# Kernel optimization log

Measured on AMD Instinct MI355X. Metric: run time of the kernel, lower is better.

The kernel has to match this reference:

```python
import jax, jax.numpy as jnp
import numpy as np

B, N, D_IN, H, D_H, D_OUT = 2, 1024, 1024, 16, 64, 1024
NEG = -1e9


def skew_relative(QE_t):
    # QE_t: [B, H, N, 2N-1] -> [B, H, N, N] via the pad/reshape skew trick
    b, h, n = QE_t.shape[0], QE_t.shape[1], QE_t.shape[2]
    x = jnp.pad(QE_t, ((0, 0), (0, 0), (0, 0), (0, 1)))          # [B,H,N,2N]
    x = x.reshape(b, h, -1)                                       # [B,H,2N^2]
    x = jnp.pad(x, ((0, 0), (0, 0), (0, n - 1)))                  # [B,H,(N+1)(2N-1)]
    x = x.reshape(b, h, n + 1, 2 * n - 1)
    return x[:, :, :n, -n:]


def setup_inputs() -> dict:
    key = jax.random.key(0)
    ks = jax.random.split(key, 8)
    x = jax.random.normal(ks[0], (B, N, D_IN), dtype=jnp.float32)
    E_rel = jax.random.normal(ks[1], (2 * N - 1, D_H), dtype=jnp.float32)
    # additive causal mask [1,1,N,N]
    causal = jnp.tril(jnp.ones((N, N), dtype=bool))
    mask = jnp.where(causal, 0.0, NEG).astype(jnp.float32)[None, None]
    s = 1.0 / np.sqrt(D_IN)
    Wq = jax.random.normal(ks[2], (D_IN, H * D_H), dtype=jnp.float32) * s
    Wk = jax.random.normal(ks[3], (D_IN, H * D_H), dtype=jnp.float32) * s
    Wv = jax.random.normal(ks[4], (D_IN, H * D_H), dtype=jnp.float32) * s
    Wo = jax.random.normal(ks[5], (H * D_H, D_OUT), dtype=jnp.float32) * (1.0 / np.sqrt(H * D_H))
    bo = jnp.zeros((D_OUT,), dtype=jnp.float32)
    return {"x": x, "E_rel": E_rel, "mask": mask, "Wq": Wq, "Wk": Wk, "Wv": Wv, "Wo": Wo, "bo": bo}


def reference(x, E_rel, mask, Wq, Wk, Wv, Wo, bo):
    b = x.shape[0]
    scale = 1.0 / np.sqrt(D_H)
    # project and split heads -> [B, H, N, d]
    Q = (x @ Wq).reshape(b, -1, H, D_H).transpose(0, 2, 1, 3)
    K = (x @ Wk).reshape(b, -1, H, D_H).transpose(0, 2, 1, 3)
    V = (x @ Wv).reshape(b, -1, H, D_H).transpose(0, 2, 1, 3)
    attn = jnp.einsum('bhnd,bhmd->bhnm', Q, K)                    # [B,H,N,N]
    QE_t = jnp.einsum('bhnd,rd->bhnr', Q, E_rel)                  # [B,H,N,2N-1]
    attn = (attn + skew_relative(QE_t)) * scale + mask
    attn = jax.nn.softmax(attn, axis=-1)
    out = jnp.einsum('bhnm,bhmd->bhnd', attn, V)                  # [B,H,N,d]
    out = out.transpose(0, 2, 1, 3).reshape(b, -1, H * D_H)
    return out @ Wo + bo  # dropout is identity at inference
```

## Files before the change

kernel.cpp:

```cpp
#include <hip/hip_runtime.h>
#include <cstdint>
#include <cstddef>

typedef __bf16 bf16;
typedef __bf16 bf16x8 __attribute__((ext_vector_type(8)));
typedef float  f32x4  __attribute__((ext_vector_type(4)));

#define MFMA16(a,b,c) __builtin_amdgcn_mfma_f32_16x16x32_bf16((a),(b),(c),0,0,0)

__device__ __forceinline__ void gload_lds16(const bf16* g, bf16* l) {
  __builtin_amdgcn_global_load_lds((__attribute__((address_space(1))) void*)(g),
                                   (__attribute__((address_space(3))) void*)(l),
                                   16, 0, 0);
}

__global__ __launch_bounds__(256) void prep_k(
    const float* __restrict__ x, const float* __restrict__ E,
    const float* __restrict__ W0, const float* __restrict__ W1,
    const float* __restrict__ W2, const float* __restrict__ W3,
    bf16* __restrict__ xb, bf16* __restrict__ Eb, bf16* __restrict__ Wt) {
  __shared__ float t[32][33];
  const int bid = blockIdx.x;
  const int tid = threadIdx.x;
  if (bid < 2176) {
    const bool isx = (bid < 2048);
    const float* src = isx ? x : E;
    bf16* dst = isx ? xb : Eb;
    const int n = isx ? (2048 * 1024) : (2047 * 64);
    const int i = (isx ? bid : (bid - 2048)) * 1024 + tid * 4;
    if (i < n) {
      float4 v = *(const float4*)(src + i);
      dst[i + 0] = (bf16)v.x;
      dst[i + 1] = (bf16)v.y;
      dst[i + 2] = (bf16)v.z;
      dst[i + 3] = (bf16)v.w;
    }
  } else {
    const int tt = bid - 2176;
    const int z = tt >> 10;
    const int rem = tt & 1023;
    const int cx = (rem & 31) * 32;
    const int ry = (rem >> 5) * 32;
    const float* src = (z == 0) ? W0 : (z == 1) ? W1 : (z == 2) ? W2 : W3;
    bf16* dst = Wt + (size_t)z * (1024 * 1024);
    const int xx = tid & 31, yy = tid >> 5;
    #pragma unroll
    for (int j = 0; j < 32; j += 8) t[yy + j][xx] = src[(size_t)(ry + yy + j) * 1024 + cx + xx];
    __syncthreads();
    #pragma unroll
    for (int j = 0; j < 32; j += 8)
      dst[(size_t)(cx + yy + j) * 1024 + ry + xx] = (bf16)t[xx][yy + j];
  }
}

template <int NI>
__global__ __launch_bounds__(256) void gemm_k(
    const bf16* __restrict__ A, const bf16* __restrict__ Bt,
    bf16* __restrict__ QKV, float* __restrict__ Of,
    const float* __restrict__ bias, const int mode) {
  constexpr int K = 1024;
  const int row0 = blockIdx.x * 64;
  const int col0 = blockIdx.y * (NI * 64);

  __shared__ bf16 As[2][64 * 64];
  __shared__ bf16 Bs[2][NI * 64 * 64];

  const int tid = threadIdx.x;
  const int lane = tid & 63;
  const int wid = tid >> 6;
  const int lr = lane & 15;
  const int g  = lane >> 4;
  const int srow = lane >> 3;
  const int scol = ((lane & 7) ^ srow) * 8;

  f32x4 acc[4][NI];
  #pragma unroll
  for (int a = 0; a < 4; ++a)
    #pragma unroll
    for (int b = 0; b < NI; ++b) acc[a][b] = (f32x4){0.f, 0.f, 0.f, 0.f};

  auto stg = [&](int bb, int k0_) {
    #pragma unroll
    for (int q = 0; q < 2; ++q)
      gload_lds16(A + (size_t)(row0 + wid * 16 + q * 8 + srow) * K + k0_ + scol,
                  &As[bb][(wid * 16 + q * 8) * 64]);
    #pragma unroll
    for (int q = 0; q < 2 * NI; ++q)
      gload_lds16(Bt + (size_t)(col0 + wid * NI * 16 + q * 8 + srow) * K + k0_ + scol,
                  &Bs[bb][(wid * NI * 16 + q * 8) * 64]);
  };

  stg(0, 0);
  for (int t = 0; t < K / 64; ++t) {
    __syncthreads();
    if (t + 1 < K / 64) stg((t + 1) & 1, (t + 1) * 64);
    const bf16* as = &As[t & 1][0];
    const bf16* bs = &Bs[t & 1][0];
    bf16x8 af[4][2], bfv[NI][2];
    #pragma unroll
    for (int mi = 0; mi < 4; ++mi)
      #pragma unroll
      for (int kk = 0; kk < 2; ++kk)
        af[mi][kk] = *(const bf16x8*)&as[(mi * 16 + lr) * 64 + ((kk * 32 + g * 8) ^ ((lr & 7) << 3))];
    #pragma unroll
    for (int ni = 0; ni < NI; ++ni)
      #pragma unroll
      for (int kk = 0; kk < 2; ++kk)
        bfv[ni][kk] = *(const bf16x8*)&bs[(wid * NI * 16 + ni * 16 + lr) * 64 +
                                          ((kk * 32 + g * 8) ^ ((lr & 7) << 3))];
    #pragma unroll
    for (int mi = 0; mi < 4; ++mi)
      #pragma unroll
      for (int ni = 0; ni < NI; ++ni)
        #pragma unroll
        for (int kk = 0; kk < 2; ++kk)
          acc[mi][ni] = MFMA16(af[mi][kk], bfv[ni][kk], acc[mi][ni]);
  }

  #pragma unroll
  for (int mi = 0; mi < 4; ++mi) {
    #pragma unroll
    for (int ni = 0; ni < NI; ++ni) {
      #pragma unroll
      for (int r = 0; r < 4; ++r) {
        const int row = row0 + mi * 16 + g * 4 + r;
        const int col = col0 + wid * NI * 16 + ni * 16 + lr;
        const float v = acc[mi][ni][r];
        if (mode == 2) {
          Of[(size_t)row * 1024 + col] = v + bias[col];
        } else {
          const int b = row >> 10, i = row & 1023;
          const int which = col >> 10, cc = col & 1023;
          const int h = cc >> 6, d = cc & 63;
          if (which < 2)
            QKV[(size_t)which * 2097152 + (((size_t)(b * 16 + h)) * 1024 + i) * 64 + d] = (bf16)v;
          else
            QKV[(size_t)2 * 2097152 + (((size_t)(b * 16 + h)) * 64 + d) * 1024 + i] = (bf16)v;
        }
      }
    }
  }
}

__device__ const int CH_QB[36] = {7,7,7,7,7,7,7, 6,6,6,6,6,6, 5,5,5,5,5, 4,4,4,4,
                                  3,3,3, 2,2, 1, 0,1,2,3,4,5,6,7};
__device__ const int CH_K0[36] = {0,2,4,6,8,10,12, 0,2,4,6,8,10, 0,2,4,6,8, 0,2,4,6,
                                  0,2,4, 0,2, 0, 0,2,4,6,8,10,12,14};
__device__ const int QB_P0[8] = {0,1,3,6,10,15,21,28};

__global__ __launch_bounds__(512, 6) void attn_kernel(
    const bf16* __restrict__ Qh, const bf16* __restrict__ Kh,
    const bf16* __restrict__ Vt, const bf16* __restrict__ Eb,
    bf16* __restrict__ OP, float* __restrict__ LP) {
  constexpr int N = 1024;
  const int flat = blockIdx.y * 36 + blockIdx.x;
  const int task = (flat & 7) * 144 + (flat >> 3);
  const int bh = task / 36;
  const int ch = task - bh * 36;
  const int qb = CH_QB[ch];
  const int kb0 = CH_K0[ch];
  const int i0 = qb * 128;

  const bf16* Qp = Qh + (size_t)bh * N * 64;
  const bf16* Kp = Kh + (size_t)bh * N * 64;
  const bf16* Vp = Vt + (size_t)bh * 64 * N;

  __shared__ bf16 Ks[64 * 64];
  __shared__ bf16 Vs[64 * 64];
  __shared__ bf16 Es[192 * 64];

  const int tid = threadIdx.x;
  const int lane = tid & 63;
  const int wid = tid >> 6;
  const int lr = lane & 15;
  const int g  = lane >> 4;
  const int iw0 = i0 + wid * 16;
  bf16* pp = &Es[(wid * 16) * 64];

  const int srow8 = lane >> 3;
  const int sch = ((lane & 7) ^ srow8) * 8;

  bf16x8 qf[2];
  {
    const bf16* qrow = Qp + (size_t)(iw0 + lr) * 64 + g * 8;
    qf[0] = *(const bf16x8*)(qrow);
    qf[1] = *(const bf16x8*)(qrow + 32);
  }

  float lb[4] = {0.f, 0.f, 0.f, 0.f};
  f32x4 oacc[4];
  #pragma unroll
  for (int r = 0; r < 4; ++r) oacc[r] = (f32x4){0.f, 0.f, 0.f, 0.f};

  constexpr float SC = 0.18033688f;
  const int fb = 7 - wid;

  auto STAGE = [&](int j0) {
    gload_lds16(Kp + (size_t)(j0 + wid * 8 + srow8) * 64 + sch, &Ks[(wid * 8) * 64]);
    gload_lds16(Vp + (size_t)(wid * 8 + srow8) * 1024 + j0 + sch, &Vs[(wid * 8) * 64]);
    const int ebase = (N - 128) + j0 - i0;
    #pragma unroll
    for (int q = 0; q < 3; ++q)
      gload_lds16(Eb + (size_t)(ebase + wid * 24 + q * 8 + srow8) * 64 + sch,
                  &Es[(wid * 24 + q * 8) * 64]);
  };

  STAGE(kb0 * 64);
  __syncthreads();

  #pragma unroll
  for (int t = 0; t < 2; ++t) {
    const int j0 = (kb0 + t) * 64;
    const bool skip = (j0 > iw0 + 15);
    float p[4][4];
    if (!skip) {
      f32x4 sa[4];
      #pragma unroll
      for (int ni = 0; ni < 4; ++ni) sa[ni] = (f32x4){0.f, 0.f, 0.f, 0.f};
      __builtin_amdgcn_s_setprio(1);
      #pragma unroll
      for (int ni = 0; ni < 4; ++ni)
        #pragma unroll
        for (int kk = 0; kk < 2; ++kk) {
          bf16x8 kf = *(const bf16x8*)&Ks[(ni * 16 + lr) * 64 +
                                          ((kk * 32 + g * 8) ^ ((lr & 7) << 3))];
          sa[ni] = MFMA16(qf[kk], kf, sa[ni]);
        }
      f32x4 ea[5];
      #pragma unroll
      for (int s5 = 0; s5 < 5; ++s5) {
        const int er = (fb + s5) * 16 + lr;
        ea[s5] = (f32x4){0.f, 0.f, 0.f, 0.f};
        bf16x8 e0 = *(const bf16x8*)&Es[er * 64 + ((g * 8) ^ ((lr & 7) << 3))];
        bf16x8 e1 = *(const bf16x8*)&Es[er * 64 + ((32 + g * 8) ^ ((lr & 7) << 3))];
        ea[s5] = MFMA16(qf[0], e0, ea[s5]);
        ea[s5] = MFMA16(qf[1], e1, ea[s5]);
      }
      __builtin_amdgcn_s_setprio(0);
      #pragma unroll
      for (int r = 0; r < 4; ++r) {
        const int di = g * 4 + r;
        const int sl = (g << 4) | ((lr - di - 1) & 15);
        const float sh0 = __shfl(ea[0][r], sl);
        const float sh1 = __shfl(ea[1][r], sl);
        const float sh2 = __shfl(ea[2][r], sl);
        const float sh3 = __shfl(ea[3][r], sl);
        const float sh4 = __shfl(ea[4][r], sl);
        const bool hi = (lr > di);
        const float rel[4] = {hi ? sh1 : sh0, hi ? sh2 : sh1, hi ? sh3 : sh2, hi ? sh4 : sh3};
        const int ig = iw0 + di;
        #pragma unroll
        for (int ni = 0; ni < 4; ++ni) {
          float tv = (sa[ni][r] + rel[ni]) * SC;
          tv = (j0 + ni * 16 + lr > ig) ? -1e30f : tv;
          const float pv = exp2f(tv);
          lb[r] += pv;
          p[ni][r] = pv;
        }
      }
    }
    __syncthreads();
    if (!skip) {
      #pragma unroll
      for (int r = 0; r < 4; ++r) {
        const int di = g * 4 + r;
        #pragma unroll
        for (int ni = 0; ni < 4; ++ni)
          pp[di * 64 + ((ni * 16 + lr) ^ ((di & 7) << 3))] = (bf16)p[ni][r];
      }
      bf16x8 pf[2];
      pf[0] = *(const bf16x8*)&pp[lr * 64 + ((g * 8) ^ ((lr & 7) << 3))];
      pf[1] = *(const bf16x8*)&pp[lr * 64 + ((32 + g * 8) ^ ((lr & 7) << 3))];
      __builtin_amdgcn_s_setprio(1);
      #pragma unroll
      for (int nd = 0; nd < 4; ++nd)
        #pragma unroll
        for (int kk = 0; kk < 2; ++kk) {
          bf16x8 vf = *(const bf16x8*)&Vs[(nd * 16 + lr) * 64 +
                                          ((kk * 32 + g * 8) ^ ((lr & 7) << 3))];
          oacc[nd] = MFMA16(pf[kk], vf, oacc[nd]);
        }
      __builtin_amdgcn_s_setprio(0);
    }
    if (t == 0) {
      __syncthreads();
      STAGE(j0 + 64);
      __syncthreads();
    }
  }

  #pragma unroll
  for (int off = 1; off < 16; off <<= 1)
    #pragma unroll
    for (int r = 0; r < 4; ++r)
      lb[r] += __shfl_xor(lb[r], off);

  const int pslot = bh * 36 + QB_P0[qb] + (kb0 >> 1);
  bf16* Op = OP + (size_t)pslot * 8192;
  #pragma unroll
  for (int nd = 0; nd < 4; ++nd)
    #pragma unroll
    for (int r = 0; r < 4; ++r)
      Op[(size_t)(wid * 16 + g * 4 + r) * 64 + nd * 16 + lr] = (bf16)oacc[nd][r];
  if (lr == 0) {
    #pragma unroll
    for (int r = 0; r < 4; ++r)
      LP[pslot * 128 + wid * 16 + g * 4 + r] = lb[r];
  }
}

__global__ __launch_bounds__(256) void merge_k(const bf16* __restrict__ OP,
                                               const float* __restrict__ LP,
                                               bf16* __restrict__ AO) {
  const int bh = blockIdx.x;
  const int qb = blockIdx.y;
  const int half = blockIdx.z;
  const int np = qb + 1;
  const int tid = threadIdx.x;
  const int row = half * 64 + (tid >> 2);
  const int c0 = (tid & 3) * 16;
  const int p0 = bh * 36 + QB_P0[qb];

  float o[16];
  #pragma unroll
  for (int j = 0; j < 16; ++j) o[j] = 0.f;
  float l = 0.f;
  for (int c = 0; c < np; ++c) {
    l += LP[(p0 + c) * 128 + row];
    const bf16* Oc = OP + (size_t)(p0 + c) * 8192 + row * 64 + c0;
    #pragma unroll
    for (int j = 0; j < 16; j += 8) {
      const bf16x8 v = *(const bf16x8*)&Oc[j];
      #pragma unroll
      for (int u = 0; u < 8; ++u) o[j + u] += (float)v[u];
    }
  }
  const float inv = 1.f / l;

  const int b = bh >> 4, h = bh & 15;
  bf16* dst = AO + ((size_t)(b * 1024) + qb * 128 + row) * 1024 + h * 64 + c0;
  #pragma unroll
  for (int j = 0; j < 16; ++j) dst[j] = (bf16)(o[j] * inv);
}

extern "C" void kernel_launch(void* const* d_in, const int* in_sizes, int n_in,
                              void* d_out, int out_size, void* d_ws, size_t ws_size,
                              hipStream_t stream) {
  const float* x  = (const float*)d_in[0];
  const float* E  = (const float*)d_in[1];
  const float* Wq = (const float*)d_in[3];
  const float* Wk = (const float*)d_in[4];
  const float* Wv = (const float*)d_in[5];
  const float* Wo = (const float*)d_in[6];
  const float* bo = (const float*)d_in[7];

  bf16* xb  = (bf16*)d_ws;
  bf16* Wqt = xb + 2048 * 1024;
  bf16* Wot = Wqt + 3 * 1024 * 1024;
  bf16* Eb  = Wqt + 4 * 1024 * 1024;
  bf16* Qh  = Eb + 2048 * 64;
  bf16* AO  = Qh + 3 * 2048 * 1024;
  bf16* OPb = AO + 2048 * 1024;
  float* LPp = (float*)(OPb + (size_t)1152 * 8192);
  float* out = (float*)d_out;

  prep_k<<<dim3(6272), dim3(256), 0, stream>>>(x, E, Wq, Wk, Wv, Wo, xb, Eb, Wqt);

  gemm_k<2><<<dim3(32, 24), dim3(256), 0, stream>>>(xb, Wqt, Qh, nullptr, nullptr, 0);

  attn_kernel<<<dim3(36, 32), dim3(512), 0, stream>>>(
      Qh, Qh + 2048 * 1024, Qh + 2 * 2048 * 1024, Eb, OPb, LPp);

  merge_k<<<dim3(32, 8, 2), dim3(256), 0, stream>>>(OPb, LPp, AO);

  gemm_k<2><<<dim3(32, 8), dim3(256), 0, stream>>>(AO, Wot, nullptr, out, bo, 2);
}
```

Measured before the change: 90.35 us.

## Double-buffer K/V in attention and move GEMMs to 512-thread 2x4 warp tiling

The attention kernel now stages both K/V tiles into separate buffers, loads the full 256-row E window once, and gives each wave its own P scratch. This lets the second tile's load overlap the first tile's compute and drops one barrier pair. Occupancy bounds drop from 6 to 4 blocks because of the larger LDS footprint. The GEMMs switch to 512-thread blocks with a 2x4 wave grid and larger tiles (128x128 for QKV, 64x128 for the output), changing per-wave reuse and the grid size.

```diff
diff --git a/kernel.cpp b/kernel.cpp
--- a/kernel.cpp
+++ b/kernel.cpp
@@ -53,41 +53,45 @@
   }
 }
 
-template <int NI>
-__global__ __launch_bounds__(256) void gemm_k(
+template <int RM, int RN>
+__global__ __launch_bounds__(512, 4) void gemm512(
     const bf16* __restrict__ A, const bf16* __restrict__ Bt,
     bf16* __restrict__ QKV, float* __restrict__ Of,
     const float* __restrict__ bias, const int mode) {
   constexpr int K = 1024;
-  const int row0 = blockIdx.x * 64;
-  const int col0 = blockIdx.y * (NI * 64);
-
-  __shared__ bf16 As[2][64 * 64];
-  __shared__ bf16 Bs[2][NI * 64 * 64];
+  constexpr int MT = 2 * RM * 16;
+  constexpr int NT = 4 * RN * 16;
+  const int row0 = blockIdx.x * MT;
+  const int col0 = blockIdx.y * NT;
+
+  __shared__ bf16 As[2][MT * 64];
+  __shared__ bf16 Bs[2][NT * 64];
 
   const int tid = threadIdx.x;
   const int lane = tid & 63;
   const int wid = tid >> 6;
+  const int wr = wid >> 2, wc = wid & 3;
   const int lr = lane & 15;
   const int g  = lane >> 4;
-  const int srow = lane >> 3;
-  const int scol = ((lane & 7) ^ srow) * 8;
-
-  f32x4 acc[4][NI];
-  #pragma unroll
-  for (int a = 0; a < 4; ++a)
-    #pragma unroll
-    for (int b = 0; b < NI; ++b) acc[a][b] = (f32x4){0.f, 0.f, 0.f, 0.f};
+  const int srow8 = lane >> 3;
+  const int scol = ((lane & 7) ^ srow8) * 8;
+
+  f32x4 acc[RM][RN];
+  #pragma unroll
+  for (int a = 0; a < RM; ++a)
+    #pragma unroll
+    for (int b = 0; b < RN; ++b) acc[a][b] = (f32x4){0.f, 0.f, 0.f, 0.f};
 
   auto stg = [&](int bb, int k0_) {
+    constexpr int ARW = MT / 8;
+    #pragma unroll
+    for (int q = 0; q < ARW / 8; ++q)
+      gload_lds16(A + (size_t)(row0 + wid * ARW + q * 8 + srow8) * K + k0_ + scol,
+                  &As[bb][(wid * ARW + q * 8) * 64]);
     #pragma unroll
     for (int q = 0; q < 2; ++q)
-      gload_lds16(A + (size_t)(row0 + wid * 16 + q * 8 + srow) * K + k0_ + scol,
-                  &As[bb][(wid * 16 + q * 8) * 64]);
-    #pragma unroll
-    for (int q = 0; q < 2 * NI; ++q)
-      gload_lds16(Bt + (size_t)(col0 + wid * NI * 16 + q * 8 + srow) * K + k0_ + scol,
-                  &Bs[bb][(wid * NI * 16 + q * 8) * 64]);
+      gload_lds16(Bt + (size_t)(col0 + wid * 16 + q * 8 + srow8) * K + k0_ + scol,
+                  &Bs[bb][(wid * 16 + q * 8) * 64]);
   };
 
   stg(0, 0);
@@ -96,35 +100,36 @@
     if (t + 1 < K / 64) stg((t + 1) & 1, (t + 1) * 64);
     const bf16* as = &As[t & 1][0];
     const bf16* bs = &Bs[t & 1][0];
-    bf16x8 af[4][2], bfv[NI][2];
-    #pragma unroll
-    for (int mi = 0; mi < 4; ++mi)
+    bf16x8 af[RM][2], bfv[RN][2];
+    #pragma unroll
+    for (int mi = 0; mi < RM; ++mi)
       #pragma unroll
       for (int kk = 0; kk < 2; ++kk)
-        af[mi][kk] = *(const bf16x8*)&as[(mi * 16 + lr) * 64 + ((kk * 32 + g * 8) ^ ((lr & 7) << 3))];
-    #pragma unroll
-    for (int ni = 0; ni < NI; ++ni)
+        af[mi][kk] = *(const bf16x8*)&as[(wr * RM * 16 + mi * 16 + lr) * 64 +
+                                         ((kk * 32 + g * 8) ^ ((lr & 7) << 3))];
+    #pragma unroll
+    for (int ni = 0; ni < RN; ++ni)
       #pragma unroll
       for (int kk = 0; kk < 2; ++kk)
-        bfv[ni][kk] = *(const bf16x8*)&bs[(wid * NI * 16 + ni * 16 + lr) * 64 +
+        bfv[ni][kk] = *(const bf16x8*)&bs[(wc * RN * 16 + ni * 16 + lr) * 64 +
                                           ((kk * 32 + g * 8) ^ ((lr & 7) << 3))];
     #pragma unroll
-    for (int mi = 0; mi < 4; ++mi)
-      #pragma unroll
-      for (int ni = 0; ni < NI; ++ni)
+    for (int mi = 0; mi < RM; ++mi)
+      #pragma unroll
+      for (int ni = 0; ni < RN; ++ni)
         #pragma unroll
         for (int kk = 0; kk < 2; ++kk)
           acc[mi][ni] = MFMA16(af[mi][kk], bfv[ni][kk], acc[mi][ni]);
   }
 
   #pragma unroll
-  for (int mi = 0; mi < 4; ++mi) {
-    #pragma unroll
-    for (int ni = 0; ni < NI; ++ni) {
+  for (int mi = 0; mi < RM; ++mi) {
+    #pragma unroll
+    for (int ni = 0; ni < RN; ++ni) {
       #pragma unroll
       for (int r = 0; r < 4; ++r) {
-        const int row = row0 + mi * 16 + g * 4 + r;
-        const int col = col0 + wid * NI * 16 + ni * 16 + lr;
+        const int row = row0 + wr * RM * 16 + mi * 16 + g * 4 + r;
+        const int col = col0 + wc * RN * 16 + ni * 16 + lr;
         const float v = acc[mi][ni][r];
         if (mode == 2) {
           Of[(size_t)row * 1024 + col] = v + bias[col];
@@ -148,7 +153,7 @@
                                   0,2,4, 0,2, 0, 0,2,4,6,8,10,12,14};
 __device__ const int QB_P0[8] = {0,1,3,6,10,15,21,28};
 
-__global__ __launch_bounds__(512, 6) void attn_kernel(
+__global__ __launch_bounds__(512, 4) void attn_kernel(
     const bf16* __restrict__ Qh, const bf16* __restrict__ Kh,
     const bf16* __restrict__ Vt, const bf16* __restrict__ Eb,
     bf16* __restrict__ OP, float* __restrict__ LP) {
@@ -165,9 +170,10 @@
   const bf16* Kp = Kh + (size_t)bh * N * 64;
   const bf16* Vp = Vt + (size_t)bh * 64 * N;
 
-  __shared__ bf16 Ks[64 * 64];
-  __shared__ bf16 Vs[64 * 64];
-  __shared__ bf16 Es[192 * 64];
+  __shared__ bf16 Ks[2][64 * 64];
+  __shared__ bf16 Vs[2][64 * 64];
+  __shared__ bf16 Es[256 * 64];
+  __shared__ bf16 Psm[8][16 * 64];
 
   const int tid = threadIdx.x;
   const int lane = tid & 63;
@@ -175,7 +181,7 @@
   const int lr = lane & 15;
   const int g  = lane >> 4;
   const int iw0 = i0 + wid * 16;
-  bf16* pp = &Es[(wid * 16) * 64];
+  bf16* pp = &Psm[wid][0];
 
   const int srow8 = lane >> 3;
   const int sch = ((lane & 7) ^ srow8) * 8;
@@ -194,100 +200,90 @@
 
   constexpr float SC = 0.18033688f;
   const int fb = 7 - wid;
-
-  auto STAGE = [&](int j0) {
-    gload_lds16(Kp + (size_t)(j0 + wid * 8 + srow8) * 64 + sch, &Ks[(wid * 8) * 64]);
-    gload_lds16(Vp + (size_t)(wid * 8 + srow8) * 1024 + j0 + sch, &Vs[(wid * 8) * 64]);
-    const int ebase = (N - 128) + j0 - i0;
-    #pragma unroll
-    for (int q = 0; q < 3; ++q)
-      gload_lds16(Eb + (size_t)(ebase + wid * 24 + q * 8 + srow8) * 64 + sch,
-                  &Es[(wid * 24 + q * 8) * 64]);
+  const int j0a = kb0 * 64;
+  const int ebase0 = (N - 128) + j0a - i0;
+
+  auto STAGE_KV = [&](int b, int j0) {
+    gload_lds16(Kp + (size_t)(j0 + wid * 8 + srow8) * 64 + sch, &Ks[b][(wid * 8) * 64]);
+    gload_lds16(Vp + (size_t)(wid * 8 + srow8) * 1024 + j0 + sch, &Vs[b][(wid * 8) * 64]);
   };
-
-  STAGE(kb0 * 64);
+  auto STAGE_E = [&]() {
+    #pragma unroll
+    for (int q = 0; q < 4; ++q)
+      gload_lds16(Eb + (size_t)(ebase0 + wid * 32 + q * 8 + srow8) * 64 + sch,
+                  &Es[(wid * 32 + q * 8) * 64]);
+  };
+
+  auto TILE = [&](int buf, int j0, int eoff) {
+    if (j0 > iw0 + 15) return;
+    const bf16* kbuf = &Ks[buf][0];
+    const bf16* vbuf = &Vs[buf][0];
+    f32x4 sa[4];
+    #pragma unroll
+    for (int ni = 0; ni < 4; ++ni) sa[ni] = (f32x4){0.f, 0.f, 0.f, 0.f};
+    __builtin_amdgcn_s_setprio(1);
+    #pragma unroll
+    for (int ni = 0; ni < 4; ++ni)
+      #pragma unroll
+      for (int kk = 0; kk < 2; ++kk) {
+        bf16x8 kf = *(const bf16x8*)&kbuf[(ni * 16 + lr) * 64 +
+                                          ((kk * 32 + g * 8) ^ ((lr & 7) << 3))];
+        sa[ni] = MFMA16(qf[kk], kf, sa[ni]);
+      }
+    f32x4 ea[5];
+    #pragma unroll
+    for (int s5 = 0; s5 < 5; ++s5) {
+      const int er = eoff + (fb + s5) * 16 + lr;
+      ea[s5] = (f32x4){0.f, 0.f, 0.f, 0.f};
+      bf16x8 e0 = *(const bf16x8*)&Es[er * 64 + ((g * 8) ^ ((lr & 7) << 3))];
+      bf16x8 e1 = *(const bf16x8*)&Es[er * 64 + ((32 + g * 8) ^ ((lr & 7) << 3))];
+      ea[s5] = MFMA16(qf[0], e0, ea[s5]);
+      ea[s5] = MFMA16(qf[1], e1, ea[s5]);
+    }
+    __builtin_amdgcn_s_setprio(0);
+    #pragma unroll
+    for (int r = 0; r < 4; ++r) {
+      const int di = g * 4 + r;
+      const int sl = (g << 4) | ((lr - di - 1) & 15);
+      const float sh0 = __shfl(ea[0][r], sl);
+      const float sh1 = __shfl(ea[1][r], sl);
+      const float sh2 = __shfl(ea[2][r], sl);
+      const float sh3 = __shfl(ea[3][r], sl);
+      const float sh4 = __shfl(ea[4][r], sl);
+      const bool hi = (lr > di);
+      const float rel[4] = {hi ? sh1 : sh0, hi ? sh2 : sh1, hi ? sh3 : sh2, hi ? sh4 : sh3};
+      const int ig = iw0 + di;
+      #pragma unroll
+      for (int ni = 0; ni < 4; ++ni) {
+        float tv = (sa[ni][r] + rel[ni]) * SC;
+        tv = (j0 + ni * 16 + lr > ig) ? -1e30f : tv;
+        const float pv = exp2f(tv);
+        lb[r] += pv;
+        pp[di * 64 + ((ni * 16 + lr) ^ ((di & 7) << 3))] = (bf16)pv;
+      }
+    }
+    bf16x8 pf[2];
+    pf[0] = *(const bf16x8*)&pp[lr * 64 + ((g * 8) ^ ((lr & 7) << 3))];
+    pf[1] = *(const bf16x8*)&pp[lr * 64 + ((32 + g * 8) ^ ((lr & 7) << 3))];
+    __builtin_amdgcn_s_setprio(1);
+    #pragma unroll
+    for (int nd = 0; nd < 4; ++nd)
+      #pragma unroll
+      for (int kk = 0; kk < 2; ++kk) {
+        bf16x8 vf = *(const bf16x8*)&vbuf[(nd * 16 + lr) * 64 +
+                                          ((kk * 32 + g * 8) ^ ((lr & 7) << 3))];
+        oacc[nd] = MFMA16(pf[kk], vf, oacc[nd]);
+      }
+    __builtin_amdgcn_s_setprio(0);
+  };
+
+  STAGE_E();
+  STAGE_KV(0, j0a);
   __syncthreads();
-
-  #pragma unroll
-  for (int t = 0; t < 2; ++t) {
-    const int j0 = (kb0 + t) * 64;
-    const bool skip = (j0 > iw0 + 15);
-    float p[4][4];
-    if (!skip) {
-      f32x4 sa[4];
-      #pragma unroll
-      for (int ni = 0; ni < 4; ++ni) sa[ni] = (f32x4){0.f, 0.f, 0.f, 0.f};
-      __builtin_amdgcn_s_setprio(1);
-      #pragma unroll
-      for (int ni = 0; ni < 4; ++ni)
-        #pragma unroll
-        for (int kk = 0; kk < 2; ++kk) {
-          bf16x8 kf = *(const bf16x8*)&Ks[(ni * 16 + lr) * 64 +
-                                          ((kk * 32 + g * 8) ^ ((lr & 7) << 3))];
-          sa[ni] = MFMA16(qf[kk], kf, sa[ni]);
-        }
-      f32x4 ea[5];
-      #pragma unroll
-      for (int s5 = 0; s5 < 5; ++s5) {
-        const int er = (fb + s5) * 16 + lr;
-        ea[s5] = (f32x4){0.f, 0.f, 0.f, 0.f};
-        bf16x8 e0 = *(const bf16x8*)&Es[er * 64 + ((g * 8) ^ ((lr & 7) << 3))];
-        bf16x8 e1 = *(const bf16x8*)&Es[er * 64 + ((32 + g * 8) ^ ((lr & 7) << 3))];
-        ea[s5] = MFMA16(qf[0], e0, ea[s5]);
-        ea[s5] = MFMA16(qf[1], e1, ea[s5]);
-      }
-      __builtin_amdgcn_s_setprio(0);
-      #pragma unroll
-      for (int r = 0; r < 4; ++r) {
-        const int di = g * 4 + r;
-        const int sl = (g << 4) | ((lr - di - 1) & 15);
-        const float sh0 = __shfl(ea[0][r], sl);
-        const float sh1 = __shfl(ea[1][r], sl);
-        const float sh2 = __shfl(ea[2][r], sl);
-        const float sh3 = __shfl(ea[3][r], sl);
-        const float sh4 = __shfl(ea[4][r], sl);
-        const bool hi = (lr > di);
-        const float rel[4] = {hi ? sh1 : sh0, hi ? sh2 : sh1, hi ? sh3 : sh2, hi ? sh4 : sh3};
-        const int ig = iw0 + di;
-        #pragma unroll
-        for (int ni = 0; ni < 4; ++ni) {
-          float tv = (sa[ni][r] + rel[ni]) * SC;
-          tv = (j0 + ni * 16 + lr > ig) ? -1e30f : tv;
-          const float pv = exp2f(tv);
-          lb[r] += pv;
-          p[ni][r] = pv;
-        }
-      }
-    }
-    __syncthreads();
-    if (!skip) {
-      #pragma unroll
-      for (int r = 0; r < 4; ++r) {
-        const int di = g * 4 + r;
-        #pragma unroll
-        for (int ni = 0; ni < 4; ++ni)
-          pp[di * 64 + ((ni * 16 + lr) ^ ((di & 7) << 3))] = (bf16)p[ni][r];
-      }
-      bf16x8 pf[2];
-      pf[0] = *(const bf16x8*)&pp[lr * 64 + ((g * 8) ^ ((lr & 7) << 3))];
-      pf[1] = *(const bf16x8*)&pp[lr * 64 + ((32 + g * 8) ^ ((lr & 7) << 3))];
-      __builtin_amdgcn_s_setprio(1);
-      #pragma unroll
-      for (int nd = 0; nd < 4; ++nd)
-        #pragma unroll
-        for (int kk = 0; kk < 2; ++kk) {
-          bf16x8 vf = *(const bf16x8*)&Vs[(nd * 16 + lr) * 64 +
-                                          ((kk * 32 + g * 8) ^ ((lr & 7) << 3))];
-          oacc[nd] = MFMA16(pf[kk], vf, oacc[nd]);
-        }
-      __builtin_amdgcn_s_setprio(0);
-    }
-    if (t == 0) {
-      __syncthreads();
-      STAGE(j0 + 64);
-      __syncthreads();
-    }
-  }
+  STAGE_KV(1, j0a + 64);
+  TILE(0, j0a, 0);
+  __syncthreads();
+  TILE(1, j0a + 64, 64);
 
   #pragma unroll
   for (int off = 1; off < 16; off <<= 1)
@@ -366,12 +362,12 @@
 
   prep_k<<<dim3(6272), dim3(256), 0, stream>>>(x, E, Wq, Wk, Wv, Wo, xb, Eb, Wqt);
 
-  gemm_k<2><<<dim3(32, 24), dim3(256), 0, stream>>>(xb, Wqt, Qh, nullptr, nullptr, 0);
+  gemm512<4, 2><<<dim3(16, 24), dim3(512), 0, stream>>>(xb, Wqt, Qh, nullptr, nullptr, 0);
 
   attn_kernel<<<dim3(36, 32), dim3(512), 0, stream>>>(
       Qh, Qh + 2048 * 1024, Qh + 2 * 2048 * 1024, Eb, OPb, LPp);
 
   merge_k<<<dim3(32, 8, 2), dim3(256), 0, stream>>>(OPb, LPp, AO);
 
-  gemm_k<2><<<dim3(32, 8), dim3(256), 0, stream>>>(AO, Wot, nullptr, out, bo, 2);
-}
+  gemm512<2, 2><<<dim3(32, 8), dim3(512), 0, stream>>>(AO, Wot, nullptr, out, bo, 2);
+}
```

Measured after the change: 83.77 us. 1.08x faster.
